# Kernel optimization log

Measured on AMD Instinct MI355X. Metric: run time of the kernel, lower is better.

Reference implementation:

```python
import jax, jax.numpy as jnp
import numpy as np
import math

D_MODEL = 1024
NUM_HEADS = 16
N_GROUP = 4
HEAD_DIM = D_MODEL // NUM_HEADS  # 64
KV_DIM = N_GROUP * HEAD_DIM      # 256
BS, SEQ = 2, 2048


def setup_inputs() -> dict:
    key = jax.random.key(0)
    ks = jax.random.split(key, 7)
    s = 0.02
    return {
        "h": jax.random.normal(ks[0], (BS, SEQ, D_MODEL), dtype=jnp.float32),
        "wq_w": jax.random.normal(ks[1], (D_MODEL, D_MODEL), dtype=jnp.float32) * s,
        "wq_b": jnp.zeros((D_MODEL,), dtype=jnp.float32),
        "wk_w": jax.random.normal(ks[2], (KV_DIM, D_MODEL), dtype=jnp.float32) * s,
        "wk_b": jnp.zeros((KV_DIM,), dtype=jnp.float32),
        "wv_w": jax.random.normal(ks[3], (KV_DIM, D_MODEL), dtype=jnp.float32) * s,
        "wv_b": jnp.zeros((KV_DIM,), dtype=jnp.float32),
    }


def reference(h, wq_w, wq_b, wk_w, wk_b, wv_w, wv_b):
    bs, seq, _ = h.shape
    rep = NUM_HEADS // N_GROUP  # heads per KV group

    # Linear projections (torch Linear: x @ W.T + b)
    q = h @ wq_w.T + wq_b                     # [bs, seq, d_model]
    k = h @ wk_w.T + wk_b                     # [bs, seq, kv_dim]
    v = h @ wv_w.T + wv_b                     # [bs, seq, kv_dim]

    q = q.reshape(bs, seq, NUM_HEADS, HEAD_DIM).transpose(0, 2, 1, 3)  # [b,H,s,d]
    k = k.reshape(bs, seq, N_GROUP, HEAD_DIM)                          # [b,s,G,d]
    v = v.reshape(bs, seq, N_GROUP, HEAD_DIM)
    # torch .repeat(1,1,1,rep).view(...,num_heads,head_dim) maps head h -> group h//rep,
    # identical to repeating each group `rep` times consecutively along the head axis.
    k = jnp.repeat(k, rep, axis=2).transpose(0, 2, 1, 3)               # [b,H,s,d]
    v = jnp.repeat(v, rep, axis=2).transpose(0, 2, 1, 3)               # [b,H,s,d]

    scores = jnp.einsum("bhqd,bhkd->bhqk", q, k) / math.sqrt(HEAD_DIM)
    attn = jax.nn.softmax(scores, axis=-1)
    out = jnp.einsum("bhqk,bhkd->bhqd", attn, v)                       # [b,H,s,d]
    out = out.transpose(0, 2, 1, 3).reshape(bs, seq, NUM_HEADS * HEAD_DIM)
    return out
```

## Files before the change

### kernel.cpp

```cpp
#include <hip/hip_runtime.h>

typedef _Float16 f16;
typedef _Float16 f16x8 __attribute__((ext_vector_type(8)));
typedef _Float16 f16x4 __attribute__((ext_vector_type(4)));
typedef float f32x4 __attribute__((ext_vector_type(4)));

#define MFMA16(a, b, c) __builtin_amdgcn_mfma_f32_16x16x32_f16((a), (b), (c), 0, 0, 0)
#define GLDS16(g, l)                                                        \
    __builtin_amdgcn_global_load_lds(                                       \
        (const __attribute__((address_space(1))) void*)(g),                 \
        (__attribute__((address_space(3))) void*)(l), 16, 0, 0)

#define SEQ 2048
#define DMODEL 1024
#define NH 16
#define NG 4
#define PAD 76

__global__ __launch_bounds__(256) void cvt_all(const float* __restrict__ h,
                                               const float* __restrict__ wq,
                                               const float* __restrict__ wk,
                                               const float* __restrict__ wv,
                                               f16* __restrict__ hb, f16* __restrict__ wqb,
                                               f16* __restrict__ wkb, f16* __restrict__ wvb) {
    const int i = blockIdx.x * 256 + threadIdx.x;
    const float* s; f16* d; int off;
    if (i < 1048576)      { s = h;  d = hb;  off = i; }
    else if (i < 1310720) { s = wq; d = wqb; off = i - 1048576; }
    else if (i < 1376256) { s = wk; d = wkb; off = i - 1310720; }
    else                  { s = wv; d = wvb; off = i - 1376256; }
    const float4 v = ((const float4*)s)[off];
    f16x4 p;
    p[0] = (f16)v.x; p[1] = (f16)v.y; p[2] = (f16)v.z; p[3] = (f16)v.w;
    ((f16x4*)d)[off] = p;
}

__global__ __launch_bounds__(256) void q_gemm(const f16* __restrict__ hA,
                                              const f16* __restrict__ W,
                                              const float* __restrict__ bias,
                                              f16* __restrict__ C,
                                              float qscale) {
    __shared__ __align__(16) f16 As[128 * 32];
    __shared__ __align__(16) f16 Bs[128 * 32];

    const int tid  = threadIdx.x;
    const int lane = tid & 63;
    const int l15  = lane & 15;
    const int l4   = lane >> 4;
    const int wave = tid >> 6;
    const int wm   = (wave >> 1) * 64;
    const int wn   = (wave & 1) * 64;
    const int m0   = blockIdx.y * 128;
    const int n0   = blockIdx.x * 128;

    const int rowA = tid >> 2;
    const int colA = (tid & 3) * 8;
    const f16* Ag = hA + (size_t)(m0 + rowA) * DMODEL + colA;
    const f16* Bg = W  + (size_t)(n0 + rowA) * DMODEL + colA;
    const int sOff = wave * 512;

    f32x4 acc[4][4];
#pragma unroll
    for (int i = 0; i < 4; i++)
#pragma unroll
        for (int j = 0; j < 4; j++) acc[i][j] = (f32x4)0.0f;

    for (int k0 = 0; k0 < DMODEL; k0 += 32) {
        GLDS16(Ag + k0,         As + sOff);
        GLDS16(Ag + 65536 + k0, As + 2048 + sOff);
        GLDS16(Bg + k0,         Bs + sOff);
        GLDS16(Bg + 65536 + k0, Bs + 2048 + sOff);
        __syncthreads();

        f16x8 af[4], bf[4];
#pragma unroll
        for (int i = 0; i < 4; i++)
            af[i] = *(const f16x8*)&As[(wm + i * 16 + l15) * 32 + l4 * 8];
#pragma unroll
        for (int j = 0; j < 4; j++)
            bf[j] = *(const f16x8*)&Bs[(wn + j * 16 + l15) * 32 + l4 * 8];
#pragma unroll
        for (int i = 0; i < 4; i++)
#pragma unroll
            for (int j = 0; j < 4; j++)
                acc[i][j] = MFMA16(af[i], bf[j], acc[i][j]);
        __syncthreads();
    }

#pragma unroll
    for (int i = 0; i < 4; i++) {
        const int mbase = m0 + wm + i * 16 + l4 * 4;
#pragma unroll
        for (int j = 0; j < 4; j++) {
            const int n  = n0 + wn + j * 16 + l15;
            const float bv = bias[n];
#pragma unroll
            for (int r = 0; r < 4; r++)
                C[(size_t)(mbase + r) * 1024 + n] = (f16)((acc[i][j][r] + bv) * qscale);
        }
    }
}

__global__ __launch_bounds__(256) void kv_gemm(const f16* __restrict__ hA,
                                               const f16* __restrict__ wk,
                                               const f16* __restrict__ wv,
                                               const float* __restrict__ bk,
                                               const float* __restrict__ bv,
                                               f16* __restrict__ Kb,
                                               f16* __restrict__ Vtb) {
    __shared__ __align__(16) f16 As[64 * 32];
    __shared__ __align__(16) f16 Bs[128 * 32];

    const int tid  = threadIdx.x;
    const int lane = tid & 63;
    const int l15  = lane & 15;
    const int l4   = lane >> 4;
    const int wave = tid >> 6;
    const int wm   = (wave >> 1) * 32;
    const int wn   = (wave & 1) * 64;
    const int bx   = blockIdx.x;
    const int m0   = blockIdx.y * 64;

    const int vmode = (bx >= 2);
    const f16* W = vmode ? wv : wk;
    const float* bias = vmode ? bv : bk;
    const int n0 = (bx & 1) * 128;

    const int rowA = tid >> 2;
    const int colA = (tid & 3) * 8;
    const f16* Ag = hA + (size_t)(m0 + rowA) * DMODEL + colA;
    const f16* Bg = W  + (size_t)(n0 + rowA) * DMODEL + colA;
    const int sOff = wave * 512;

    f32x4 acc[2][4];
#pragma unroll
    for (int i = 0; i < 2; i++)
#pragma unroll
        for (int j = 0; j < 4; j++) acc[i][j] = (f32x4)0.0f;

    for (int k0 = 0; k0 < DMODEL; k0 += 32) {
        GLDS16(Ag + k0,         As + sOff);
        GLDS16(Bg + k0,         Bs + sOff);
        GLDS16(Bg + 65536 + k0, Bs + 2048 + sOff);
        __syncthreads();

        f16x8 af[2], bf[4];
#pragma unroll
        for (int i = 0; i < 2; i++)
            af[i] = *(const f16x8*)&As[(wm + i * 16 + l15) * 32 + l4 * 8];
#pragma unroll
        for (int j = 0; j < 4; j++)
            bf[j] = *(const f16x8*)&Bs[(wn + j * 16 + l15) * 32 + l4 * 8];
#pragma unroll
        for (int i = 0; i < 2; i++)
#pragma unroll
            for (int j = 0; j < 4; j++)
                acc[i][j] = MFMA16(af[i], bf[j], acc[i][j]);
        __syncthreads();
    }

#pragma unroll
    for (int i = 0; i < 2; i++) {
        const int mbase = m0 + wm + i * 16 + l4 * 4;
#pragma unroll
        for (int j = 0; j < 4; j++) {
            const int n  = n0 + wn + j * 16 + l15;
            const float bvv = bias[n];
            if (!vmode) {
#pragma unroll
                for (int r = 0; r < 4; r++)
                    Kb[(size_t)(mbase + r) * 256 + n] = (f16)(acc[i][j][r] + bvv);
            } else {
                f16x4 p;
#pragma unroll
                for (int r = 0; r < 4; r++)
                    p[r] = (f16)(acc[i][j][r] + bvv);
                const int bb = mbase >> 11;
                const int s  = mbase & 2047;
                *(f16x4*)&Vtb[((size_t)(bb * 256 + n)) * SEQ + s] = p;
            }
        }
    }
}

__global__ __launch_bounds__(256, 4) void attn_kernel(const f16* __restrict__ Q,
                                                      const f16* __restrict__ Kt,
                                                      const f16* __restrict__ Vt,
                                                      float* __restrict__ out) {
    __shared__ __align__(16) f16 Ks[64 * PAD];
    __shared__ __align__(16) f16 Vs[64 * PAD];
    __shared__ __align__(16) f16 Ps[64 * PAD];

    const int tid  = threadIdx.x;
    const int lane = tid & 63;
    const int l15  = lane & 15;
    const int l4   = lane >> 4;
    const int wave = tid >> 6;
    const int b    = blockIdx.z;
    const int hh   = blockIdx.y;
    const int g    = hh >> 2;
    const int q0   = blockIdx.x * 64;
    const int qw   = wave * 16;

    f16x8 qf[2];
#pragma unroll
    for (int kt = 0; kt < 2; kt++)
        qf[kt] = *(const f16x8*)&Q[((size_t)(b * SEQ + q0 + qw + l15)) * DMODEL + hh * 64 + kt * 32 + l4 * 8];

    f32x4 oacc[4];
    float lsum[4];
#pragma unroll
    for (int dt = 0; dt < 4; dt++) oacc[dt] = (f32x4)0.0f;
#pragma unroll
    for (int r = 0; r < 4; r++) lsum[r] = 0.0f;

    const int srow = tid >> 2;
    const int sc8  = (tid & 3) * 8;
    const f16* Kg = Kt + (size_t)(b * SEQ + srow) * 256 + g * 64 + sc8;
    const f16* Vg = Vt + (size_t)(b * 256 + g * 64 + srow) * SEQ + sc8;

    for (int kb = 0; kb < SEQ; kb += 64) {
        *(f16x8*)&Ks[srow * PAD + sc8]      = *(const f16x8*)(Kg + (size_t)kb * 256);
        *(f16x8*)&Ks[srow * PAD + 32 + sc8] = *(const f16x8*)(Kg + (size_t)kb * 256 + 32);
        *(f16x8*)&Vs[srow * PAD + sc8]      = *(const f16x8*)(Vg + kb);
        *(f16x8*)&Vs[srow * PAD + 32 + sc8] = *(const f16x8*)(Vg + kb + 32);
        __syncthreads();

        f32x4 sacc[4];
#pragma unroll
        for (int jt = 0; jt < 4; jt++) sacc[jt] = (f32x4)0.0f;
#pragma unroll
        for (int jt = 0; jt < 4; jt++) {
            const f16x8 kf0 = *(const f16x8*)&Ks[(jt * 16 + l15) * PAD + l4 * 8];
            const f16x8 kf1 = *(const f16x8*)&Ks[(jt * 16 + l15) * PAD + 32 + l4 * 8];
            sacc[jt] = MFMA16(qf[0], kf0, sacc[jt]);
            sacc[jt] = MFMA16(qf[1], kf1, sacc[jt]);
        }

#pragma unroll
        for (int jt = 0; jt < 4; jt++)
#pragma unroll
            for (int r = 0; r < 4; r++) {
                const float p = exp2f(sacc[jt][r]);
                lsum[r] += p;
                Ps[(qw + l4 * 4 + r) * PAD + jt * 16 + l15] = (f16)p;
            }

#pragma unroll
        for (int kt = 0; kt < 2; kt++) {
            const f16x8 pf = *(const f16x8*)&Ps[(qw + l15) * PAD + kt * 32 + l4 * 8];
#pragma unroll
            for (int dt = 0; dt < 4; dt++) {
                const f16x8 vf = *(const f16x8*)&Vs[(dt * 16 + l15) * PAD + kt * 32 + l4 * 8];
                oacc[dt] = MFMA16(pf, vf, oacc[dt]);
            }
        }
        __syncthreads();
    }

#pragma unroll
    for (int r = 0; r < 4; r++) {
        float l = lsum[r];
        l += __shfl_xor(l, 1);
        l += __shfl_xor(l, 2);
        l += __shfl_xor(l, 4);
        l += __shfl_xor(l, 8);
        const float inv = 1.0f / l;
        const int q = q0 + qw + l4 * 4 + r;
        float* op = out + ((size_t)(b * SEQ + q)) * DMODEL + hh * 64;
#pragma unroll
        for (int dt = 0; dt < 4; dt++)
            op[dt * 16 + l15] = oacc[dt][r] * inv;
    }
}

extern "C" void kernel_launch(void* const* d_in, const int* in_sizes, int n_in,
                              void* d_out, int out_size, void* d_ws, size_t ws_size,
                              hipStream_t stream) {
    const float* h    = (const float*)d_in[0];
    const float* wq_w = (const float*)d_in[1];
    const float* wq_b = (const float*)d_in[2];
    const float* wk_w = (const float*)d_in[3];
    const float* wk_b = (const float*)d_in[4];
    const float* wv_w = (const float*)d_in[5];
    const float* wv_b = (const float*)d_in[6];
    float* out = (float*)d_out;

    char* ws = (char*)d_ws;
    f16* hb  = (f16*)(ws + 0);
    f16* wqb = (f16*)(ws + 8388608);
    f16* wkb = (f16*)(ws + 10485760);
    f16* wvb = (f16*)(ws + 11010048);
    f16* Qb  = (f16*)(ws + 11534336);
    f16* Kb  = (f16*)(ws + 19922944);
    f16* Vtb = (f16*)(ws + 22020096);

    cvt_all<<<5632, 256, 0, stream>>>(h, wq_w, wk_w, wv_w, hb, wqb, wkb, wvb);

    const float qscale = 0.125f * 1.4426950408889634f;
    q_gemm<<<dim3(8, 32), 256, 0, stream>>>(hb, wqb, wq_b, Qb, qscale);
    kv_gemm<<<dim3(4, 64), 256, 0, stream>>>(hb, wkb, wvb, wk_b, wv_b, Kb, Vtb);

    attn_kernel<<<dim3(32, 16, 2), 256, 0, stream>>>(Qb, Kb, Vtb, out);
}
```

Before: 202.8 us.

## Fuse Q projection into attention kernel prologue, drop separate Q GEMM

```diff
diff --git a/kernel.cpp b/kernel.cpp
--- a/kernel.cpp
+++ b/kernel.cpp
@@ -16,6 +16,7 @@
 #define NH 16
 #define NG 4
 #define PAD 76
+#define QTP 68
 
 __global__ __launch_bounds__(256) void cvt_all(const float* __restrict__ h,
                                                const float* __restrict__ wq,
@@ -35,72 +36,6 @@
     ((f16x4*)d)[off] = p;
 }
 
-__global__ __launch_bounds__(256) void q_gemm(const f16* __restrict__ hA,
-                                              const f16* __restrict__ W,
-                                              const float* __restrict__ bias,
-                                              f16* __restrict__ C,
-                                              float qscale) {
-    __shared__ __align__(16) f16 As[128 * 32];
-    __shared__ __align__(16) f16 Bs[128 * 32];
-
-    const int tid  = threadIdx.x;
-    const int lane = tid & 63;
-    const int l15  = lane & 15;
-    const int l4   = lane >> 4;
-    const int wave = tid >> 6;
-    const int wm   = (wave >> 1) * 64;
-    const int wn   = (wave & 1) * 64;
-    const int m0   = blockIdx.y * 128;
-    const int n0   = blockIdx.x * 128;
-
-    const int rowA = tid >> 2;
-    const int colA = (tid & 3) * 8;
-    const f16* Ag = hA + (size_t)(m0 + rowA) * DMODEL + colA;
-    const f16* Bg = W  + (size_t)(n0 + rowA) * DMODEL + colA;
-    const int sOff = wave * 512;
-
-    f32x4 acc[4][4];
-#pragma unroll
-    for (int i = 0; i < 4; i++)
-#pragma unroll
-        for (int j = 0; j < 4; j++) acc[i][j] = (f32x4)0.0f;
-
-    for (int k0 = 0; k0 < DMODEL; k0 += 32) {
-        GLDS16(Ag + k0,         As + sOff);
-        GLDS16(Ag + 65536 + k0, As + 2048 + sOff);
-        GLDS16(Bg + k0,         Bs + sOff);
-        GLDS16(Bg + 65536 + k0, Bs + 2048 + sOff);
-        __syncthreads();
-
-        f16x8 af[4], bf[4];
-#pragma unroll
-        for (int i = 0; i < 4; i++)
-            af[i] = *(const f16x8*)&As[(wm + i * 16 + l15) * 32 + l4 * 8];
-#pragma unroll
-        for (int j = 0; j < 4; j++)
-            bf[j] = *(const f16x8*)&Bs[(wn + j * 16 + l15) * 32 + l4 * 8];
-#pragma unroll
-        for (int i = 0; i < 4; i++)
-#pragma unroll
-            for (int j = 0; j < 4; j++)
-                acc[i][j] = MFMA16(af[i], bf[j], acc[i][j]);
-        __syncthreads();
-    }
-
-#pragma unroll
-    for (int i = 0; i < 4; i++) {
-        const int mbase = m0 + wm + i * 16 + l4 * 4;
-#pragma unroll
-        for (int j = 0; j < 4; j++) {
-            const int n  = n0 + wn + j * 16 + l15;
-            const float bv = bias[n];
-#pragma unroll
-            for (int r = 0; r < 4; r++)
-                C[(size_t)(mbase + r) * 1024 + n] = (f16)((acc[i][j][r] + bv) * qscale);
-        }
-    }
-}
-
 __global__ __launch_bounds__(256) void kv_gemm(const f16* __restrict__ hA,
                                                const f16* __restrict__ wk,
                                                const f16* __restrict__ wv,
@@ -183,13 +118,17 @@
     }
 }
 
-__global__ __launch_bounds__(256, 4) void attn_kernel(const f16* __restrict__ Q,
+__global__ __launch_bounds__(256, 4) void attn_kernel(const f16* __restrict__ hb,
+                                                      const f16* __restrict__ wqb,
+                                                      const float* __restrict__ bq,
                                                       const f16* __restrict__ Kt,
                                                       const f16* __restrict__ Vt,
-                                                      float* __restrict__ out) {
+                                                      float* __restrict__ out,
+                                                      float qscale) {
     __shared__ __align__(16) f16 Ks[64 * PAD];
     __shared__ __align__(16) f16 Vs[64 * PAD];
     __shared__ __align__(16) f16 Ps[64 * PAD];
+    __shared__ __align__(16) f16 Qt[64 * QTP];
 
     const int tid  = threadIdx.x;
     const int lane = tid & 63;
@@ -202,10 +141,50 @@
     const int q0   = blockIdx.x * 64;
     const int qw   = wave * 16;
 
+    {
+        const int rowT = tid >> 2;
+        const int colT = (tid & 3) * 16;
+        const f16* Hg = hb  + (size_t)(b * SEQ + q0 + rowT) * DMODEL + colT;
+        const f16* Wg = wqb + (size_t)(hh * 64 + rowT) * DMODEL + colT;
+
+        f32x4 qacc[4];
+#pragma unroll
+        for (int j = 0; j < 4; j++) qacc[j] = (f32x4)0.0f;
+
+        for (int k0 = 0; k0 < DMODEL; k0 += 64) {
+            __syncthreads();
+            *(f16x8*)&Ks[rowT * PAD + colT]     = *(const f16x8*)(Hg + k0);
+            *(f16x8*)&Ks[rowT * PAD + colT + 8] = *(const f16x8*)(Hg + k0 + 8);
+            *(f16x8*)&Vs[rowT * PAD + colT]     = *(const f16x8*)(Wg + k0);
+            *(f16x8*)&Vs[rowT * PAD + colT + 8] = *(const f16x8*)(Wg + k0 + 8);
+            __syncthreads();
+
+#pragma unroll
+            for (int kc = 0; kc < 2; kc++) {
+                const f16x8 af = *(const f16x8*)&Ks[(qw + l15) * PAD + kc * 32 + l4 * 8];
+#pragma unroll
+                for (int j = 0; j < 4; j++) {
+                    const f16x8 bf = *(const f16x8*)&Vs[(j * 16 + l15) * PAD + kc * 32 + l4 * 8];
+                    qacc[j] = MFMA16(af, bf, qacc[j]);
+                }
+            }
+        }
+
+#pragma unroll
+        for (int j = 0; j < 4; j++) {
+            const float bv = bq[hh * 64 + j * 16 + l15];
+#pragma unroll
+            for (int r = 0; r < 4; r++)
+                Qt[(qw + l4 * 4 + r) * QTP + j * 16 + l15] = (f16)((qacc[j][r] + bv) * qscale);
+        }
+    }
+
     f16x8 qf[2];
 #pragma unroll
     for (int kt = 0; kt < 2; kt++)
-        qf[kt] = *(const f16x8*)&Q[((size_t)(b * SEQ + q0 + qw + l15)) * DMODEL + hh * 64 + kt * 32 + l4 * 8];
+        qf[kt] = *(const f16x8*)&Qt[(qw + l15) * QTP + kt * 32 + l4 * 8];
+
+    __syncthreads();
 
     f32x4 oacc[4];
     float lsum[4];
@@ -291,15 +270,13 @@
     f16* wqb = (f16*)(ws + 8388608);
     f16* wkb = (f16*)(ws + 10485760);
     f16* wvb = (f16*)(ws + 11010048);
-    f16* Qb  = (f16*)(ws + 11534336);
-    f16* Kb  = (f16*)(ws + 19922944);
-    f16* Vtb = (f16*)(ws + 22020096);
+    f16* Kb  = (f16*)(ws + 11534336);
+    f16* Vtb = (f16*)(ws + 13631488);
 
     cvt_all<<<5632, 256, 0, stream>>>(h, wq_w, wk_w, wv_w, hb, wqb, wkb, wvb);
 
+    kv_gemm<<<dim3(4, 64), 256, 0, stream>>>(hb, wkb, wvb, wk_b, wv_b, Kb, Vtb);
+
     const float qscale = 0.125f * 1.4426950408889634f;
-    q_gemm<<<dim3(8, 32), 256, 0, stream>>>(hb, wqb, wq_b, Qb, qscale);
-    kv_gemm<<<dim3(4, 64), 256, 0, stream>>>(hb, wkb, wvb, wk_b, wv_b, Kb, Vtb);
-
-    attn_kernel<<<dim3(32, 16, 2), 256, 0, stream>>>(Qb, Kb, Vtb, out);
-}
+    attn_kernel<<<dim3(32, 16, 2), 256, 0, stream>>>(hb, wqb, wq_b, Kb, Vtb, out, qscale);
+}
```

New measurement: 194.2 us. 1.04x faster.
